# Kernel optimization log

Hardware: AMD Instinct MI355X
Metric: run time of the kernel (lower is better)

The kernel has to match this reference:

```python
import jax, jax.numpy as jnp
import numpy as np

ALPHA = 0.2  # LeakyReLU negative slope
NEG_INF = -9e15


def setup_inputs() -> dict:
    key = jax.random.key(0)
    k1, k2, k3, k4, k5 = jax.random.split(key, 5)
    N, F_in, F_out = 8192, 128, 64
    h = jax.random.normal(k1, (N, F_in), dtype=jnp.float32)
    adj = jax.random.randint(k2, (N, N), 0, 2, dtype=jnp.int32)
    edge_feat = jax.random.normal(k3, (N, N), dtype=jnp.float32)
    W = jax.random.normal(k4, (F_in, F_out), dtype=jnp.float32) * 0.1
    a = jax.random.normal(k5, (2 * F_out + 1, 1), dtype=jnp.float32) * 0.1
    return {"h": h, "adj": adj, "edge_feat": edge_feat, "W": W, "a": a}


def reference(h, adj, edge_feat, W, a):
    # Wh: [N, F']
    Wh = h @ W
    F_out = W.shape[1]
    # Decompose the linear score over the concatenated features:
    # e[i,j] = leakyrelu( Wh[i].a1 + Wh[j].a2 + edge_feat[i,j]*a_e )
    a1 = a[:F_out, 0]          # applied to source (row i) features
    a2 = a[F_out:2 * F_out, 0]  # applied to target (col j) features
    a_e = a[2 * F_out, 0]       # applied to scalar edge feature
    s1 = Wh @ a1               # [N]
    s2 = Wh @ a2               # [N]
    e = s1[:, None] + s2[None, :] + edge_feat * a_e  # [N, N]
    e = jnp.where(e > 0, e, ALPHA * e)  # LeakyReLU
    e = jnp.where(adj > 0, e, NEG_INF)
    attention = jax.nn.softmax(e, axis=1)  # [N, N]
    h_prime = attention @ Wh               # [N, F']
    return jax.nn.elu(h_prime)
```

## Files before the change

kernel.cpp:

```cpp
#include <hip/hip_runtime.h>
#include <hip/hip_bf16.h>

#define N_NODES 8192
#define F_IN    128
#define F_OUT   64
#define GAT_ALPHA 0.2f
#define JSPLIT  16
#define COLS_PER_SPLIT (N_NODES / JSPLIT)
#define KC      64
#define NCH     (COLS_PER_SPLIT / KC)
#define LSTR    72

typedef short  short8_t  __attribute__((ext_vector_type(8)));
typedef float  f32x4_t   __attribute__((ext_vector_type(4)));

static __device__ __forceinline__ unsigned int f32_to_bf16_bits(float x) {
    unsigned int u = __float_as_uint(x);
    return (u + 0x7fffu + ((u >> 16) & 1u)) >> 16;
}

__global__ __launch_bounds__(256) void k_wh(
    const float* __restrict__ h, const float* __restrict__ W, const float* __restrict__ a,
    unsigned short* __restrict__ wht, float* __restrict__ s1, float* __restrict__ s2)
{
    __shared__ float Wl[F_IN][F_OUT];
    int tid = threadIdx.x;
    #pragma unroll
    for (int i = 0; i < (F_IN * F_OUT) / 256; ++i) {
        int idx = tid + i * 256;
        Wl[idx >> 6][idx & 63] = W[idx];
    }
    __syncthreads();
    int wave = tid >> 6, lane = tid & 63;
    int row = blockIdx.x * 4 + wave;
    const float* hr = h + (size_t)row * F_IN;
    float acc = 0.f;
    #pragma unroll
    for (int k = 0; k < F_IN; k += 4) {
        float4 hv = *(const float4*)(hr + k);
        acc += hv.x * Wl[k + 0][lane];
        acc += hv.y * Wl[k + 1][lane];
        acc += hv.z * Wl[k + 2][lane];
        acc += hv.w * Wl[k + 3][lane];
    }
    wht[(size_t)lane * N_NODES + row] = (unsigned short)f32_to_bf16_bits(acc);
    float p1 = acc * a[lane];
    float p2 = acc * a[F_OUT + lane];
    #pragma unroll
    for (int off = 32; off > 0; off >>= 1) {
        p1 += __shfl_down(p1, off);
        p2 += __shfl_down(p2, off);
    }
    if (lane == 0) { s1[row] = p1; s2[row] = p2; }
}

__global__ __launch_bounds__(256) void k_attn(
    const int* __restrict__ adj, const float* __restrict__ ef,
    const float* __restrict__ a,
    const float* __restrict__ s1, const float* __restrict__ s2,
    const unsigned short* __restrict__ wht,
    float* __restrict__ Osum, float* __restrict__ lsum)
{
    __shared__ unsigned short pl[4 * 2 * 16 * LSTR];
    int tid  = threadIdx.x;
    int wave = tid >> 6, lane = tid & 63;
    int q = lane >> 4, m = lane & 15;
    int r  = lane >> 2;
    int cq = lane & 3;
    int rowtile = blockIdx.x / JSPLIT;
    int split   = blockIdx.x % JSPLIT;
    int row0  = rowtile * 64 + wave * 16;
    int jbase = split * COLS_PER_SPLIT;

    float a_e = a[2 * F_OUT];
    int Rr = row0 + r;
    float s1v = s1[Rr];
    const int*   adjr = adj + (size_t)Rr * N_NODES + jbase + cq * 16;
    const float* efr  = ef  + (size_t)Rr * N_NODES + jbase + cq * 16;
    const float* s2r  = s2 + jbase + cq * 16;
    unsigned short* plw = pl + wave * (2 * 16 * LSTR);
    const unsigned short* wm = wht + (size_t)m * N_NODES + jbase;

    f32x4_t acc0 = {0.f, 0.f, 0.f, 0.f};
    f32x4_t acc1 = acc0, acc2 = acc0, acc3 = acc0, accl = acc0;
    short8_t ones;
    #pragma unroll
    for (int i = 0; i < 8; ++i) ones[i] = (short)0x3F80;

    int4   aj[4];
    float4 ev[4], sv[4];
    #pragma unroll
    for (int u = 0; u < 4; ++u) {
        aj[u] = *(const int4*)  (adjr + u * 4);
        ev[u] = *(const float4*)(efr  + u * 4);
        sv[u] = *(const float4*)(s2r  + u * 4);
    }

    #pragma unroll 2
    for (int ch = 0; ch < NCH; ++ch) {
        const unsigned short* wp = wm + ch * KC + q * 8;
        short8_t b[8];
        #pragma unroll
        for (int kk = 0; kk < 2; ++kk)
            #pragma unroll
            for (int t = 0; t < 4; ++t)
                b[kk * 4 + t] = *(const short8_t*)(wp + (size_t)t * 16 * N_NODES + kk * 32);

        uint2 pk[4];
        #pragma unroll
        for (int u = 0; u < 4; ++u) {
            float e0 = fmaf(ev[u].x, a_e, s1v + sv[u].x); e0 = fmaxf(e0, GAT_ALPHA * e0);
            float e1 = fmaf(ev[u].y, a_e, s1v + sv[u].y); e1 = fmaxf(e1, GAT_ALPHA * e1);
            float e2 = fmaf(ev[u].z, a_e, s1v + sv[u].z); e2 = fmaxf(e2, GAT_ALPHA * e2);
            float e3 = fmaf(ev[u].w, a_e, s1v + sv[u].w); e3 = fmaxf(e3, GAT_ALPHA * e3);
            float p0 = (aj[u].x > 0) ? __expf(e0) : 0.f;
            float p1 = (aj[u].y > 0) ? __expf(e1) : 0.f;
            float p2 = (aj[u].z > 0) ? __expf(e2) : 0.f;
            float p3 = (aj[u].w > 0) ? __expf(e3) : 0.f;
            pk[u].x = f32_to_bf16_bits(p0) | (f32_to_bf16_bits(p1) << 16);
            pk[u].y = f32_to_bf16_bits(p2) | (f32_to_bf16_bits(p3) << 16);
        }

        if (ch + 1 < NCH) {
            adjr += KC; efr += KC; s2r += KC;
            #pragma unroll
            for (int u = 0; u < 4; ++u) {
                aj[u] = *(const int4*)  (adjr + u * 4);
                ev[u] = *(const float4*)(efr  + u * 4);
                sv[u] = *(const float4*)(s2r  + u * 4);
            }
        }

        unsigned short* pb = plw + (ch & 1) * (16 * LSTR);
        #pragma unroll
        for (int u = 0; u < 4; ++u)
            *(uint2*)&pb[r * LSTR + cq * 16 + u * 4] = pk[u];

        const unsigned short* pr = pb + m * LSTR;
        #pragma unroll
        for (int kk = 0; kk < 2; ++kk) {
            short8_t af = *(const short8_t*)&pr[kk * 32 + q * 8];
            acc0 = __builtin_amdgcn_mfma_f32_16x16x32_bf16(af, b[kk * 4 + 0], acc0, 0, 0, 0);
            acc1 = __builtin_amdgcn_mfma_f32_16x16x32_bf16(af, b[kk * 4 + 1], acc1, 0, 0, 0);
            acc2 = __builtin_amdgcn_mfma_f32_16x16x32_bf16(af, b[kk * 4 + 2], acc2, 0, 0, 0);
            acc3 = __builtin_amdgcn_mfma_f32_16x16x32_bf16(af, b[kk * 4 + 3], acc3, 0, 0, 0);
            accl = __builtin_amdgcn_mfma_f32_16x16x32_bf16(af, ones, accl, 0, 0, 0);
        }
    }

    #pragma unroll
    for (int rr = 0; rr < 4; ++rr) {
        int orow = row0 + q * 4 + rr;
        float* op = Osum + (size_t)orow * F_OUT + m;
        atomicAdd(op +  0, acc0[rr]);
        atomicAdd(op + 16, acc1[rr]);
        atomicAdd(op + 32, acc2[rr]);
        atomicAdd(op + 48, acc3[rr]);
    }
    if (m == 0) {
        #pragma unroll
        for (int rr = 0; rr < 4; ++rr)
            atomicAdd(&lsum[row0 + q * 4 + rr], accl[rr]);
    }
}

__global__ __launch_bounds__(256) void k_out(
    const float* __restrict__ Osum, const float* __restrict__ lsum, float* __restrict__ out)
{
    int i = blockIdx.x * 256 + threadIdx.x;
    float v = Osum[i] / lsum[i >> 6];
    out[i] = (v > 0.f) ? v : (__expf(v) - 1.f);
}

extern "C" void kernel_launch(void* const* d_in, const int* in_sizes, int n_in,
                              void* d_out, int out_size, void* d_ws, size_t ws_size,
                              hipStream_t stream)
{
    const float* h   = (const float*)d_in[0];
    const int*   adj = (const int*)d_in[1];
    const float* ef  = (const float*)d_in[2];
    const float* W   = (const float*)d_in[3];
    const float* a   = (const float*)d_in[4];
    float* out = (float*)d_out;

    char* ws = (char*)d_ws;
    unsigned short* wht = (unsigned short*)ws;
    float* s1   = (float*)(ws + (size_t)F_OUT * N_NODES * 2);
    float* s2   = s1 + N_NODES;
    float* Osum = s2 + N_NODES;
    float* lsum = Osum + (size_t)N_NODES * F_OUT;

    hipMemsetAsync(Osum, 0, ((size_t)N_NODES * F_OUT + N_NODES) * sizeof(float), stream);

    k_wh  <<<N_NODES / 4, 256, 0, stream>>>(h, W, a, wht, s1, s2);
    k_attn<<<(N_NODES / 64) * JSPLIT, 256, 0, stream>>>(adj, ef, a, s1, s2, wht, Osum, lsum);
    k_out <<<(N_NODES * F_OUT) / 256, 256, 0, stream>>>(Osum, lsum, out);
}
```

Measured before the change: 551.1 us.

## Pre-swizzle Wh into MFMA fragment layout and coalesce adj/edge loads

The Wh projection kernel now writes bf16 Wh in a blocked layout matching the MFMA B-fragment order, so each lane in the attention kernel loads its eight B fragments as contiguous 16-byte chunks instead of strided loads across 16 rows of N. The attention kernel also remaps lanes so 16 consecutive lanes read consecutive 4-element groups of one adj/edge_feat row (four rows per lane), giving fully coalesced 256-byte row segments. The LDS write pattern and s1 handling change to match. The main cost targeted is poor memory coalescing on the streamed N×N inputs and the Wh operand.

```diff
diff --git a/kernel.cpp b/kernel.cpp
--- a/kernel.cpp
+++ b/kernel.cpp
@@ -43,7 +43,12 @@
         acc += hv.z * Wl[k + 2][lane];
         acc += hv.w * Wl[k + 3][lane];
     }
-    wht[(size_t)lane * N_NODES + row] = (unsigned short)f32_to_bf16_bits(acc);
+    int c  = row & 63, cb = row >> 6;
+    int u  = ((c >> 5) << 2) + (lane >> 4);
+    int lp = (((c >> 3) & 3) << 4) + (lane & 15);
+    wht[(size_t)cb * 4096 + u * 512 + lp * 8 + (c & 7)] =
+        (unsigned short)f32_to_bf16_bits(acc);
+
     float p1 = acc * a[lane];
     float p2 = acc * a[F_OUT + lane];
     #pragma unroll
@@ -65,21 +70,22 @@
     int tid  = threadIdx.x;
     int wave = tid >> 6, lane = tid & 63;
     int q = lane >> 4, m = lane & 15;
-    int r  = lane >> 2;
-    int cq = lane & 3;
+    int rg = q, sg = m;
     int rowtile = blockIdx.x / JSPLIT;
     int split   = blockIdx.x % JSPLIT;
     int row0  = rowtile * 64 + wave * 16;
     int jbase = split * COLS_PER_SPLIT;
 
     float a_e = a[2 * F_OUT];
-    int Rr = row0 + r;
-    float s1v = s1[Rr];
-    const int*   adjr = adj + (size_t)Rr * N_NODES + jbase + cq * 16;
-    const float* efr  = ef  + (size_t)Rr * N_NODES + jbase + cq * 16;
-    const float* s2r  = s2 + jbase + cq * 16;
+    float s1v[4];
+    #pragma unroll
+    for (int t = 0; t < 4; ++t) s1v[t] = s1[row0 + t * 4 + rg];
+
+    const int*   adjp = adj + (size_t)(row0 + rg) * N_NODES + jbase + sg * 4;
+    const float* efp  = ef  + (size_t)(row0 + rg) * N_NODES + jbase + sg * 4;
+    const float* s2p  = s2 + jbase + sg * 4;
+    const unsigned short* w3 = wht + (size_t)(split * NCH) * 4096 + lane * 8;
     unsigned short* plw = pl + wave * (2 * 16 * LSTR);
-    const unsigned short* wm = wht + (size_t)m * N_NODES + jbase;
 
     f32x4_t acc0 = {0.f, 0.f, 0.f, 0.f};
     f32x4_t acc1 = acc0, acc2 = acc0, acc3 = acc0, accl = acc0;
@@ -87,54 +93,55 @@
     #pragma unroll
     for (int i = 0; i < 8; ++i) ones[i] = (short)0x3F80;
 
+    const size_t RSTR = (size_t)4 * N_NODES;
+
     int4   aj[4];
-    float4 ev[4], sv[4];
-    #pragma unroll
-    for (int u = 0; u < 4; ++u) {
-        aj[u] = *(const int4*)  (adjr + u * 4);
-        ev[u] = *(const float4*)(efr  + u * 4);
-        sv[u] = *(const float4*)(s2r  + u * 4);
-    }
+    float4 ev[4], sv;
+    #pragma unroll
+    for (int t = 0; t < 4; ++t) {
+        aj[t] = *(const int4*)  (adjp + t * RSTR);
+        ev[t] = *(const float4*)(efp  + t * RSTR);
+    }
+    sv = *(const float4*)s2p;
 
     #pragma unroll 2
     for (int ch = 0; ch < NCH; ++ch) {
-        const unsigned short* wp = wm + ch * KC + q * 8;
+        const unsigned short* wt = w3 + (size_t)ch * 4096;
         short8_t b[8];
         #pragma unroll
-        for (int kk = 0; kk < 2; ++kk)
+        for (int u = 0; u < 8; ++u)
+            b[u] = *(const short8_t*)(wt + u * 512);
+
+        uint2 pk[4];
+        #pragma unroll
+        for (int t = 0; t < 4; ++t) {
+            float sb = s1v[t];
+            float e0 = fmaf(ev[t].x, a_e, sb + sv.x); e0 = fmaxf(e0, GAT_ALPHA * e0);
+            float e1 = fmaf(ev[t].y, a_e, sb + sv.y); e1 = fmaxf(e1, GAT_ALPHA * e1);
+            float e2 = fmaf(ev[t].z, a_e, sb + sv.z); e2 = fmaxf(e2, GAT_ALPHA * e2);
+            float e3 = fmaf(ev[t].w, a_e, sb + sv.w); e3 = fmaxf(e3, GAT_ALPHA * e3);
+            float p0 = (aj[t].x > 0) ? __expf(e0) : 0.f;
+            float p1 = (aj[t].y > 0) ? __expf(e1) : 0.f;
+            float p2 = (aj[t].z > 0) ? __expf(e2) : 0.f;
+            float p3 = (aj[t].w > 0) ? __expf(e3) : 0.f;
+            pk[t].x = f32_to_bf16_bits(p0) | (f32_to_bf16_bits(p1) << 16);
+            pk[t].y = f32_to_bf16_bits(p2) | (f32_to_bf16_bits(p3) << 16);
+        }
+
+        if (ch + 1 < NCH) {
+            adjp += KC; efp += KC; s2p += KC;
             #pragma unroll
-            for (int t = 0; t < 4; ++t)
-                b[kk * 4 + t] = *(const short8_t*)(wp + (size_t)t * 16 * N_NODES + kk * 32);
-
-        uint2 pk[4];
-        #pragma unroll
-        for (int u = 0; u < 4; ++u) {
-            float e0 = fmaf(ev[u].x, a_e, s1v + sv[u].x); e0 = fmaxf(e0, GAT_ALPHA * e0);
-            float e1 = fmaf(ev[u].y, a_e, s1v + sv[u].y); e1 = fmaxf(e1, GAT_ALPHA * e1);
-            float e2 = fmaf(ev[u].z, a_e, s1v + sv[u].z); e2 = fmaxf(e2, GAT_ALPHA * e2);
-            float e3 = fmaf(ev[u].w, a_e, s1v + sv[u].w); e3 = fmaxf(e3, GAT_ALPHA * e3);
-            float p0 = (aj[u].x > 0) ? __expf(e0) : 0.f;
-            float p1 = (aj[u].y > 0) ? __expf(e1) : 0.f;
-            float p2 = (aj[u].z > 0) ? __expf(e2) : 0.f;
-            float p3 = (aj[u].w > 0) ? __expf(e3) : 0.f;
-            pk[u].x = f32_to_bf16_bits(p0) | (f32_to_bf16_bits(p1) << 16);
-            pk[u].y = f32_to_bf16_bits(p2) | (f32_to_bf16_bits(p3) << 16);
+            for (int t = 0; t < 4; ++t) {
+                aj[t] = *(const int4*)  (adjp + t * RSTR);
+                ev[t] = *(const float4*)(efp  + t * RSTR);
+            }
+            sv = *(const float4*)s2p;
         }
 
-        if (ch + 1 < NCH) {
-            adjr += KC; efr += KC; s2r += KC;
-            #pragma unroll
-            for (int u = 0; u < 4; ++u) {
-                aj[u] = *(const int4*)  (adjr + u * 4);
-                ev[u] = *(const float4*)(efr  + u * 4);
-                sv[u] = *(const float4*)(s2r  + u * 4);
-            }
-        }
-
         unsigned short* pb = plw + (ch & 1) * (16 * LSTR);
         #pragma unroll
-        for (int u = 0; u < 4; ++u)
-            *(uint2*)&pb[r * LSTR + cq * 16 + u * 4] = pk[u];
+        for (int t = 0; t < 4; ++t)
+            *(uint2*)&pb[(t * 4 + rg) * LSTR + sg * 4] = pk[t];
 
         const unsigned short* pr = pb + m * LSTR;
         #pragma unroll
```

Result: no change. 540.6 us (-1.9%).
